# Kernel tuning notes

Measured on AMD Instinct MI355X. Metric: run time of the kernel, lower is better.

The kernel has to match this reference:

```python
import jax, jax.numpy as jnp
import numpy as np

B, L, H, N, CIN, COUT, U = 32, 12, 12, 2048, 2, 1, 64
K3 = 3  # num_matrices = n_supports * max_diffusion_step + 1 = 1*2 + 1


def setup_inputs() -> dict:
    rng = np.random.default_rng(0)
    # random sparse-ish symmetric adjacency -> scaled laplacian support (lambda_max ~= 2)
    A = rng.random((N, N), dtype=np.float32)
    A = np.maximum(A, A.T)
    A = A * (A > 0.995)
    d = A.sum(axis=1)
    dis = 1.0 / np.sqrt(np.maximum(d, 1e-6))
    Lap = np.eye(N, dtype=np.float32) - (dis[:, None] * A) * dis[None, :]
    support = (Lap - np.eye(N, dtype=np.float32)).astype(np.float32)  # 2/lmax*L - I with lmax=2

    key = jax.random.key(0)
    ks = jax.random.split(key, 6)

    def w(k, shape, fan):
        return jax.random.normal(k, shape, jnp.float32) / np.float32(np.sqrt(fan))

    Cg_e = (CIN + U) * K3   # 198
    Cg_d = (COUT + U) * K3  # 195
    return {
        "history_data": jax.random.normal(ks[0], (B, L, N, CIN), jnp.float32),
        "support": jnp.asarray(support),
        "enc_Wg": w(ks[1], (Cg_e, 2 * U), Cg_e),
        "enc_bg": jnp.ones((2 * U,), jnp.float32),  # gate bias starts at 1.0 (original repo)
        "enc_Wc": w(ks[2], (Cg_e, U), Cg_e),
        "enc_bc": jnp.zeros((U,), jnp.float32),
        "dec_Wg": w(ks[3], (Cg_d, 2 * U), Cg_d),
        "dec_bg": jnp.ones((2 * U,), jnp.float32),
        "dec_Wc": w(ks[4], (Cg_d, U), Cg_d),
        "dec_bc": jnp.zeros((U,), jnp.float32),
        "Wp": w(ks[5], (U, COUT), U),
        "bp": jnp.zeros((COUT,), jnp.float32),
    }


def _gconv(support, x, W, b):
    # x: [B, N, C]; Chebyshev diffusion T0=x, T1=Sx, T2=2S(Sx)-x, stacked feature-major
    x1 = jnp.einsum('mn,bnc->bmc', support, x)
    x2 = 2.0 * jnp.einsum('mn,bnc->bmc', support, x1) - x
    xs = jnp.stack([x, x1, x2], axis=-1)  # [B, N, C, 3]
    b_, n_, c_, k_ = xs.shape
    y = xs.reshape(b_ * n_, c_ * k_) @ W + b
    return y.reshape(b_, n_, -1)


def _cell(support, x, h, Wg, bg, Wc, bc):
    # DCGRU cell: x [B,N,in], h [B,N,U]
    cat = jnp.concatenate([x, h], axis=-1)
    ru = jax.nn.sigmoid(_gconv(support, cat, Wg, bg))
    r, u = jnp.split(ru, 2, axis=-1)
    c = jnp.tanh(_gconv(support, jnp.concatenate([x, r * h], axis=-1), Wc, bc))
    return u * h + (1.0 - u) * c


def reference(history_data, support, enc_Wg, enc_bg, enc_Wc, enc_bc,
              dec_Wg, dec_bg, dec_Wc, dec_bc, Wp, bp):
    hist = jnp.transpose(history_data, (1, 0, 2, 3))  # [L, B, N, CIN]
    h0 = jnp.zeros((B, N, U), history_data.dtype)

    def enc_step(h, xt):
        return _cell(support, xt, h, enc_Wg, enc_bg, enc_Wc, enc_bc), None

    h_enc, _ = jax.lax.scan(enc_step, h0, hist)

    go = jnp.zeros((B, N, COUT), history_data.dtype)

    def dec_step(carry, _):
        h, xin = carry
        h = _cell(support, xin, h, dec_Wg, dec_bg, dec_Wc, dec_bc)
        out = (h.reshape(-1, U) @ Wp + bp).reshape(B, N, COUT)
        return (h, out), out

    _, outs = jax.lax.scan(dec_step, (h_enc, go), None, length=H)  # [H, B, N, COUT]
    return jnp.transpose(outs, (1, 0, 2, 3))  # [B, H, N, COUT]
```

## Files before the change

### kernel.cpp

```cpp
#include <hip/hip_runtime.h>
#include <math.h>

#define NN 2048
#define BB 32
#define LL 12
#define HHH 12
#define UU 64
#define STR 68
#define SLAB (BB*STR)
#define SEGS 8
#define SEGW (SLAB/SEGS)
#define MR (NN*BB)
#define CSR_CAP 262144
#define PACK_HALF 28672

typedef short bfrag __attribute__((ext_vector_type(8)));
typedef float ffrag __attribute__((ext_vector_type(4)));

__device__ __forceinline__ float sigm(float x) { return 1.0f / (1.0f + __expf(-x)); }
__device__ __forceinline__ float tanhfast(float x) {
  float e = __expf(2.0f * x);
  return 1.0f - 2.0f / (e + 1.0f);
}

__device__ __forceinline__ void cvt8(const float* a, bfrag* hi, bfrag* lo) {
  bfrag H, L;
  #pragma unroll
  for (int j = 0; j < 8; ++j) {
    unsigned u = __float_as_uint(a[j]);
    unsigned hb = (u + 0x7FFFu + ((u >> 16) & 1u)) >> 16;
    float rem = a[j] - __uint_as_float(hb << 16);
    unsigned u2 = __float_as_uint(rem);
    unsigned lb = (u2 + 0x7FFFu + ((u2 >> 16) & 1u)) >> 16;
    H[j] = (short)hb; L[j] = (short)lb;
  }
  *hi = H; *lo = L;
}

__global__ __launch_bounds__(256) void k_row_count(const float* __restrict__ S, int* __restrict__ cnt) {
  int m = blockIdx.x;
  const float* row = S + (size_t)m * NN;
  int c = 0;
  for (int i = threadIdx.x; i < NN; i += 256) c += (row[i] != 0.0f);
  __shared__ int sm[4];
  for (int off = 32; off; off >>= 1) c += __shfl_down(c, off, 64);
  if ((threadIdx.x & 63) == 0) sm[threadIdx.x >> 6] = c;
  __syncthreads();
  if (threadIdx.x == 0) cnt[m] = sm[0] + sm[1] + sm[2] + sm[3];
}

__global__ __launch_bounds__(256) void k_scan(const int* __restrict__ cnt, int* __restrict__ rp) {
  __shared__ int tot[256];
  int t = threadIdx.x;
  int base = t * 8;
  int v[8]; int s = 0;
  #pragma unroll
  for (int k = 0; k < 8; ++k) { v[k] = cnt[base + k]; s += v[k]; }
  tot[t] = s;
  __syncthreads();
  for (int off = 1; off < 256; off <<= 1) {
    int add = (t >= off) ? tot[t - off] : 0;
    __syncthreads();
    tot[t] += add;
    __syncthreads();
  }
  int run = (t == 0) ? 0 : tot[t - 1];
  #pragma unroll
  for (int k = 0; k < 8; ++k) { rp[base + k] = run; run += v[k]; }
  if (t == 255) rp[NN] = run;
}

__global__ __launch_bounds__(256) void k_fill(const float* __restrict__ S, const int* __restrict__ rp,
                                              int* __restrict__ cols, float* __restrict__ vals) {
  int m = blockIdx.x;
  const float* row = S + (size_t)m * NN;
  __shared__ int wsum[4];
  __shared__ int chunkbase;
  if (threadIdx.x == 0) chunkbase = rp[m];
  __syncthreads();
  int lane = threadIdx.x & 63, w = threadIdx.x >> 6;
  for (int ch = 0; ch < NN / 256; ++ch) {
    int i = ch * 256 + threadIdx.x;
    float val = row[i];
    bool p = (val != 0.0f);
    unsigned long long mask = __ballot(p);
    int rank = __popcll(mask & ((1ull << lane) - 1ull));
    if (lane == 0) wsum[w] = __popcll(mask);
    __syncthreads();
    int off = 0;
    for (int q = 0; q < w; ++q) off += wsum[q];
    if (p) { int k = chunkbase + off + rank; cols[k] = i * SLAB; vals[k] = val; }
    __syncthreads();
    if (threadIdx.x == 0) chunkbase += wsum[0] + wsum[1] + wsum[2] + wsum[3];
    __syncthreads();
  }
}

__global__ __launch_bounds__(256) void k_pack(const float* __restrict__ Wsrc, unsigned short* __restrict__ dst,
                                              int CIN_, int NO) {
  int idx = blockIdx.x * 256 + threadIdx.x;
  int nh_count = NO >> 6;
  int tot = nh_count * 7 * 4 * 64 * 8;
  if (idx >= tot) return;
  int j = idx & 7;
  int r1 = idx >> 3;  int lane = r1 & 63;
  int r2 = r1 >> 6;   int nf = r2 & 3;
  int r3 = r2 >> 2;   int ks = r3 % 7; int nh = r3 / 7;
  int grp = lane >> 4, l15 = lane & 15;
  int col = nh*64 + nf*16 + l15;
  float wv = 0.0f;
  int kb = -1, c = 0;
  if (ks < 6) {
    kb = ks >> 1;
    c = CIN_ + (ks & 1)*32 + grp*8 + j;
  } else {
    int q = grp*8 + j;
    if (q < 3*CIN_) { kb = q / CIN_; c = q % CIN_; }
  }
  if (kb >= 0) {
    float w0 = Wsrc[((size_t)c*3 + 0)*NO + col];
    float w1 = Wsrc[((size_t)c*3 + 1)*NO + col];
    float w2 = Wsrc[((size_t)c*3 + 2)*NO + col];
    wv = (kb == 0) ? (w0 - w2) : ((kb == 1) ? w1 : 2.0f*w2);
  }
  unsigned u = __float_as_uint(wv);
  unsigned hb = (u + 0x7FFFu + ((u >> 16) & 1u)) >> 16;
  float rem = wv - __uint_as_float(hb << 16);
  unsigned u2 = __float_as_uint(rem);
  unsigned lb = (u2 + 0x7FFFu + ((u2 >> 16) & 1u)) >> 16;
  size_t basehi = ((size_t)nh*PACK_HALF) + ((((size_t)ks*4 + nf)*2 + 0)*64 + lane)*8 + j;
  size_t baselo = ((size_t)nh*PACK_HALF) + ((((size_t)ks*4 + nf)*2 + 1)*64 + lane)*8 + j;
  dst[basehi] = (unsigned short)hb;
  dst[baselo] = (unsigned short)lb;
}

__global__ __launch_bounds__(256) void k_setx(const float* __restrict__ hist, float* __restrict__ cat, int t) {
  int idx = blockIdx.x * 256 + threadIdx.x;
  if (idx >= MR * 2) return;
  int c = idx & 1, row = idx >> 1;
  int n = row >> 5, b = row & 31;
  cat[(size_t)row * STR + 64 + c] = hist[(((size_t)(b * LL + t)) * NN + n) * 2 + c];
}

__global__ __launch_bounds__(320) void k_hop(
    const int* __restrict__ rp, const int* __restrict__ colsS, const float* __restrict__ vals,
    const float* __restrict__ src, float* __restrict__ Y) {
  int orig = blockIdx.x;
  int swz = (orig & 7) * 2048 + (orig >> 3);
  int seg = swz >> 11;
  int node = swz & 2047;
  int tid = threadIdx.x;
  if (tid >= SEGW) return;
  int w0 = seg * SEGW + tid;
  int j0 = rp[node], j1 = rp[node + 1];
  float acc0 = 0.f, acc1 = 0.f;
  int j = j0;
  for (; j + 4 <= j1; j += 4) {
    int   o0 = colsS[j],   o1 = colsS[j+1], o2 = colsS[j+2], o3 = colsS[j+3];
    float s0 = vals[j],    s1 = vals[j+1],  s2 = vals[j+2],  s3 = vals[j+3];
    float v0 = src[o0 + w0];
    float v1 = src[o1 + w0];
    float v2 = src[o2 + w0];
    float v3 = src[o3 + w0];
    acc0 = fmaf(s0, v0, acc0);
    acc1 = fmaf(s1, v1, acc1);
    acc0 = fmaf(s2, v2, acc0);
    acc1 = fmaf(s3, v3, acc1);
  }
  for (; j < j1; ++j) acc0 = fmaf(vals[j], src[colsS[j] + w0], acc0);
  Y[(size_t)node * SLAB + w0] = acc0 + acc1;
}

template<int CATM>
__global__ __launch_bounds__(256, 4) void k_gate(
    const float* __restrict__ catP, const float* __restrict__ T1P, const float* __restrict__ T2P,
    const unsigned short* __restrict__ Bpack, const float* __restrict__ bg,
    float* __restrict__ zP, float* __restrict__ Ug) {
  int tid = threadIdx.x;
  int r0 = blockIdx.x * 64;
  int w = tid >> 6, lane = tid & 63, grp = lane >> 4, l15 = lane & 15;
  int row0 = r0 + w*16 + l15;
  ffrag acc[8];
  #pragma unroll
  for (int nf = 0; nf < 8; ++nf) acc[nf] = (ffrag){0.f, 0.f, 0.f, 0.f};

  #pragma unroll
  for (int ks = 0; ks < 7; ++ks) {
    int ko = (ks & 1)*32 + grp*8;
    float av[8] = {0,0,0,0,0,0,0,0};
    if (ks < 6) {
      const float* p0 = (ks < 2) ? catP : ((ks < 4) ? T1P : T2P);
      const float* a0 = p0 + (size_t)row0*STR + ko;
      *(float4*)(av)     = *(const float4*)a0;
      *(float4*)(av + 4) = *(const float4*)(a0 + 4);
    } else if (grp == 0) {
      size_t rb = (size_t)row0*STR + 64;
      if (CATM == 1) {
        av[0] = catP[rb];  av[1] = catP[rb + 1];
        av[2] = T1P[rb];   av[3] = T1P[rb + 1];
        av[4] = T2P[rb];   av[5] = T2P[rb + 1];
      } else {
        av[0] = catP[rb];
        av[1] = T1P[rb];
        av[2] = T2P[rb];
      }
    }
    bfrag ah0, al0;
    cvt8(av, &ah0, &al0);
    #pragma unroll
    for (int nf = 0; nf < 8; ++nf) {
      const unsigned short* bb = Bpack + (size_t)(nf >> 2)*PACK_HALF
                               + (((size_t)(ks*4 + (nf & 3))*2)*64 + lane)*8;
      bfrag bh = *(const bfrag*)bb;
      bfrag bl = *(const bfrag*)(bb + 512);
      acc[nf] = __builtin_amdgcn_mfma_f32_16x16x32_bf16(ah0, bh, acc[nf], 0, 0, 0);
      acc[nf] = __builtin_amdgcn_mfma_f32_16x16x32_bf16(ah0, bl, acc[nf], 0, 0, 0);
      acc[nf] = __builtin_amdgcn_mfma_f32_16x16x32_bf16(al0, bh, acc[nf], 0, 0, 0);
    }
  }
  float bgv[8];
  #pragma unroll
  for (int nf = 0; nf < 8; ++nf) bgv[nf] = bg[nf*16 + l15];
  #pragma unroll
  for (int reg = 0; reg < 4; ++reg) {
    int row = r0 + w*16 + grp*4 + reg;
    #pragma unroll
    for (int nf = 0; nf < 8; ++nf) {
      int col = nf*16 + l15;
      float v = sigm(acc[nf][reg] + bgv[nf]);
      if (col < 64) {
        float ho = catP[(size_t)row*STR + col];
        zP[(size_t)row*STR + col] = v * ho;
      } else {
        Ug[(size_t)row*UU + (col - 64)] = v;
      }
    }
  }
  if (l15 == 0) {
    #pragma unroll
    for (int reg = 0; reg < 4; ++reg) {
      int row = r0 + w*16 + grp*4 + reg;
      size_t zb = (size_t)row*STR;
      zP[zb + 64] = catP[zb + 64];
      zP[zb + 65] = (CATM == 1) ? catP[zb + 65] : 0.f;
      zP[zb + 66] = 0.f; zP[zb + 67] = 0.f;
    }
  }
}

template<bool DEC>
__global__ __launch_bounds__(256, 4) void k_cand(
    const float* __restrict__ zP, const float* __restrict__ T1P, const float* __restrict__ T2P,
    const unsigned short* __restrict__ Bpack, const float* __restrict__ bc,
    const float* __restrict__ Ug, const float* __restrict__ catCur,
    float* __restrict__ catNext,
    const float* __restrict__ Wp, const float* __restrict__ bp,
    float* __restrict__ out, int t) {
  int tid = threadIdx.x;
  int r0 = blockIdx.x * 64;
  int w = tid >> 6, lane = tid & 63, grp = lane >> 4, l15 = lane & 15;
  int row0 = r0 + w*16 + l15;
  ffrag acc[4];
  #pragma unroll
  for (int nf = 0; nf < 4; ++nf) acc[nf] = (ffrag){0.f, 0.f, 0.f, 0.f};

  #pragma unroll
  for (int ks = 0; ks < 7; ++ks) {
    int ko = (ks & 1)*32 + grp*8;
    float av[8] = {0,0,0,0,0,0,0,0};
    if (ks < 6) {
      const float* p0 = (ks < 2) ? zP : ((ks < 4) ? T1P : T2P);
      const float* a0 = p0 + (size_t)row0*STR + ko;
      *(float4*)(av)     = *(const float4*)a0;
      *(float4*)(av + 4) = *(const float4*)(a0 + 4);
    } else if (grp == 0) {
      size_t rb = (size_t)row0*STR + 64;
      if (!DEC) {
        av[0] = zP[rb];  av[1] = zP[rb + 1];
        av[2] = T1P[rb]; av[3] = T1P[rb + 1];
        av[4] = T2P[rb]; av[5] = T2P[rb + 1];
      } else {
        av[0] = zP[rb];
        av[1] = T1P[rb];
        av[2] = T2P[rb];
      }
    }
    bfrag ah0, al0;
    cvt8(av, &ah0, &al0);
    #pragma unroll
    for (int nf = 0; nf < 4; ++nf) {
      const unsigned short* bb = Bpack + (((size_t)(ks*4 + nf)*2)*64 + lane)*8;
      bfrag bh = *(const bfrag*)bb;
      bfrag bl = *(const bfrag*)(bb + 512);
      acc[nf] = __builtin_amdgcn_mfma_f32_16x16x32_bf16(ah0, bh, acc[nf], 0, 0, 0);
      acc[nf] = __builtin_amdgcn_mfma_f32_16x16x32_bf16(ah0, bl, acc[nf], 0, 0, 0);
      acc[nf] = __builtin_amdgcn_mfma_f32_16x16x32_bf16(al0, bh, acc[nf], 0, 0, 0);
    }
  }
  float bcv[4], wpv[4];
  #pragma unroll
  for (int nf = 0; nf < 4; ++nf) {
    bcv[nf] = bc[nf*16 + l15];
    wpv[nf] = DEC ? Wp[nf*16 + l15] : 0.f;
  }
  float bp0 = DEC ? bp[0] : 0.f;
  #pragma unroll
  for (int reg = 0; reg < 4; ++reg) {
    int row = r0 + w*16 + grp*4 + reg;
    float p = 0.f;
    #pragma unroll
    for (int nf = 0; nf < 4; ++nf) {
      int col = nf*16 + l15;
      float cf = tanhfast(acc[nf][reg] + bcv[nf]);
      float u  = Ug[(size_t)row*UU + col];
      float ho = catCur[(size_t)row*STR + col];
      float hv = u * ho + (1.0f - u) * cf;
      catNext[(size_t)row*STR + col] = hv;
      if (DEC) p = fmaf(hv, wpv[nf], p);
    }
    if (DEC) {
      p += __shfl_xor(p, 1, 64);
      p += __shfl_xor(p, 2, 64);
      p += __shfl_xor(p, 4, 64);
      p += __shfl_xor(p, 8, 64);
      if (l15 == 0) {
        float val = p + bp0;
        int n = row >> 5, b = row & 31;
        out[((size_t)b*HHH + t)*NN + n] = val;
        catNext[(size_t)row*STR + 64] = val;
        catNext[(size_t)row*STR + 65] = 0.f;
      }
    } else {
      if (l15 == 0) {
        catNext[(size_t)row*STR + 64] = 0.f;
        catNext[(size_t)row*STR + 65] = 0.f;
      }
    }
  }
}

extern "C" void kernel_launch(void* const* d_in, const int* in_sizes, int n_in,
                              void* d_out, int out_size, void* d_ws, size_t ws_size,
                              hipStream_t stream) {
  (void)in_sizes; (void)n_in; (void)out_size; (void)ws_size;
  const float* hist = (const float*)d_in[0];
  const float* support = (const float*)d_in[1];
  const float* eWg = (const float*)d_in[2];
  const float* ebg = (const float*)d_in[3];
  const float* eWc = (const float*)d_in[4];
  const float* ebc = (const float*)d_in[5];
  const float* dWg = (const float*)d_in[6];
  const float* dbg = (const float*)d_in[7];
  const float* dWc = (const float*)d_in[8];
  const float* dbc = (const float*)d_in[9];
  const float* Wp  = (const float*)d_in[10];
  const float* bp  = (const float*)d_in[11];
  float* out = (float*)d_out;

  char* base = (char*)d_ws;
  size_t off = 0;
  auto carve = [&](size_t bytes) -> void* {
    void* p = base + off;
    off += (bytes + 255) & ~(size_t)255;
    return p;
  };
  int*   cnt   = (int*)carve(NN * 4);
  int*   rpB   = (int*)carve((NN + 1) * 4);
  int*   colsB = (int*)carve(CSR_CAP * 4);
  float* valsB = (float*)carve(CSR_CAP * 4);
  unsigned short* Pge = (unsigned short*)carve(2 * PACK_HALF * 2);
  unsigned short* Pgd = (unsigned short*)carve(2 * PACK_HALF * 2);
  unsigned short* Pce = (unsigned short*)carve((size_t)PACK_HALF * 2);
  unsigned short* Pcd = (unsigned short*)carve((size_t)PACK_HALF * 2);
  float* T1P  = (float*)carve((size_t)NN * SLAB * 4);
  float* T2P  = (float*)carve((size_t)NN * SLAB * 4);
  float* zP   = (float*)carve((size_t)NN * SLAB * 4);
  float* UgF  = (float*)carve((size_t)MR * UU * 4);
  float* catA = (float*)carve((size_t)NN * SLAB * 4);
  float* catB = (float*)carve((size_t)NN * SLAB * 4);

  hipMemsetAsync(catA, 0, (size_t)NN * SLAB * 4, stream);
  hipMemsetAsync(catB, 0, (size_t)NN * SLAB * 4, stream);

  k_row_count<<<NN, 256, 0, stream>>>(support, cnt);
  k_scan<<<1, 256, 0, stream>>>(cnt, rpB);
  k_fill<<<NN, 256, 0, stream>>>(support, rpB, colsB, valsB);
  k_pack<<<112, 256, 0, stream>>>(eWg, Pge, 2, 128);
  k_pack<<<56, 256, 0, stream>>>(eWc, Pce, 2, 64);
  k_pack<<<112, 256, 0, stream>>>(dWg, Pgd, 1, 128);
  k_pack<<<56, 256, 0, stream>>>(dWc, Pcd, 1, 64);

  float* hc = catA; float* hn = catB;
  for (int t = 0; t < LL; ++t) {
    k_setx<<<(MR*2 + 255)/256, 256, 0, stream>>>(hist, hc, t);
    k_hop<<<NN*SEGS, 320, 0, stream>>>(rpB, colsB, valsB, hc, T1P);
    k_hop<<<NN*SEGS, 320, 0, stream>>>(rpB, colsB, valsB, T1P, T2P);
    k_gate<1><<<MR/64, 256, 0, stream>>>(hc, T1P, T2P, Pge, ebg, zP, UgF);
    k_hop<<<NN*SEGS, 320, 0, stream>>>(rpB, colsB, valsB, zP, T1P);
    k_hop<<<NN*SEGS, 320, 0, stream>>>(rpB, colsB, valsB, T1P, T2P);
    k_cand<false><<<MR/64, 256, 0, stream>>>(zP, T1P, T2P, Pce, ebc, UgF, hc, hn,
                                             Wp, bp, out, t);
    float* tmp = hc; hc = hn; hn = tmp;
  }
  for (int t = 0; t < HHH; ++t) {
    k_hop<<<NN*SEGS, 320, 0, stream>>>(rpB, colsB, valsB, hc, T1P);
    k_hop<<<NN*SEGS, 320, 0, stream>>>(rpB, colsB, valsB, T1P, T2P);
    k_gate<2><<<MR/64, 256, 0, stream>>>(hc, T1P, T2P, Pgd, dbg, zP, UgF);
    k_hop<<<NN*SEGS, 320, 0, stream>>>(rpB, colsB, valsB, zP, T1P);
    k_hop<<<NN*SEGS, 320, 0, stream>>>(rpB, colsB, valsB, T1P, T2P);
    k_cand<true><<<MR/64, 256, 0, stream>>>(zP, T1P, T2P, Pcd, dbc, UgF, hc, hn,
                                            Wp, bp, out, t);
    float* tmp = hc; hc = hn; hn = tmp;
  }
}
```

Before: 4.489 ms.

## Stage weights in LDS, split gate columns, pair nodes in hop, fuse setx

The gate and candidate GEMM kernels now copy the packed bf16 weight halves into shared memory once per 512-thread block, and the gate kernel splits its 128 output columns across two blocks. Each hop block now processes two nodes, with their gather loops interleaved. The per-step input-copy kernel is removed: the encoder candidate kernel writes the next step's history features directly. Together these aim to cut global weight re-reads, launch count and per-block overhead, at the cost of a 56KB LDS footprint that limits occupancy and more imbalanced hop work.

```diff
diff --git a/kernel.cpp b/kernel.cpp
--- a/kernel.cpp
+++ b/kernel.cpp
@@ -146,43 +146,72 @@
     const int* __restrict__ rp, const int* __restrict__ colsS, const float* __restrict__ vals,
     const float* __restrict__ src, float* __restrict__ Y) {
   int orig = blockIdx.x;
-  int swz = (orig & 7) * 2048 + (orig >> 3);
-  int seg = swz >> 11;
-  int node = swz & 2047;
+  int seg = orig & 7;
+  int pair = orig >> 3;
+  int nodeA = pair * 2, nodeB = nodeA + 1;
   int tid = threadIdx.x;
   if (tid >= SEGW) return;
   int w0 = seg * SEGW + tid;
-  int j0 = rp[node], j1 = rp[node + 1];
-  float acc0 = 0.f, acc1 = 0.f;
-  int j = j0;
-  for (; j + 4 <= j1; j += 4) {
-    int   o0 = colsS[j],   o1 = colsS[j+1], o2 = colsS[j+2], o3 = colsS[j+3];
-    float s0 = vals[j],    s1 = vals[j+1],  s2 = vals[j+2],  s3 = vals[j+3];
-    float v0 = src[o0 + w0];
-    float v1 = src[o1 + w0];
-    float v2 = src[o2 + w0];
-    float v3 = src[o3 + w0];
-    acc0 = fmaf(s0, v0, acc0);
-    acc1 = fmaf(s1, v1, acc1);
-    acc0 = fmaf(s2, v2, acc0);
-    acc1 = fmaf(s3, v3, acc1);
-  }
-  for (; j < j1; ++j) acc0 = fmaf(vals[j], src[colsS[j] + w0], acc0);
-  Y[(size_t)node * SLAB + w0] = acc0 + acc1;
+  int ja = rp[nodeA], ja1 = rp[nodeA + 1];
+  int jb = rp[nodeB], jb1 = rp[nodeB + 1];
+  float accA0 = 0.f, accA1 = 0.f, accB0 = 0.f, accB1 = 0.f;
+
+  while (ja + 4 <= ja1 && jb + 4 <= jb1) {
+    int   oa0 = colsS[ja],   oa1 = colsS[ja+1], oa2 = colsS[ja+2], oa3 = colsS[ja+3];
+    int   ob0 = colsS[jb],   ob1 = colsS[jb+1], ob2 = colsS[jb+2], ob3 = colsS[jb+3];
+    float sa0 = vals[ja],    sa1 = vals[ja+1],  sa2 = vals[ja+2],  sa3 = vals[ja+3];
+    float sb0 = vals[jb],    sb1 = vals[jb+1],  sb2 = vals[jb+2],  sb3 = vals[jb+3];
+    float va0 = src[oa0 + w0], va1 = src[oa1 + w0], va2 = src[oa2 + w0], va3 = src[oa3 + w0];
+    float vb0 = src[ob0 + w0], vb1 = src[ob1 + w0], vb2 = src[ob2 + w0], vb3 = src[ob3 + w0];
+    accA0 = fmaf(sa0, va0, accA0); accA1 = fmaf(sa1, va1, accA1);
+    accA0 = fmaf(sa2, va2, accA0); accA1 = fmaf(sa3, va3, accA1);
+    accB0 = fmaf(sb0, vb0, accB0); accB1 = fmaf(sb1, vb1, accB1);
+    accB0 = fmaf(sb2, vb2, accB0); accB1 = fmaf(sb3, vb3, accB1);
+    ja += 4; jb += 4;
+  }
+  for (; ja + 4 <= ja1; ja += 4) {
+    int   o0 = colsS[ja],  o1 = colsS[ja+1], o2 = colsS[ja+2], o3 = colsS[ja+3];
+    float s0 = vals[ja],   s1 = vals[ja+1],  s2 = vals[ja+2],  s3 = vals[ja+3];
+    float v0 = src[o0 + w0], v1 = src[o1 + w0], v2 = src[o2 + w0], v3 = src[o3 + w0];
+    accA0 = fmaf(s0, v0, accA0); accA1 = fmaf(s1, v1, accA1);
+    accA0 = fmaf(s2, v2, accA0); accA1 = fmaf(s3, v3, accA1);
+  }
+  for (; ja < ja1; ++ja) accA0 = fmaf(vals[ja], src[colsS[ja] + w0], accA0);
+  for (; jb + 4 <= jb1; jb += 4) {
+    int   o0 = colsS[jb],  o1 = colsS[jb+1], o2 = colsS[jb+2], o3 = colsS[jb+3];
+    float s0 = vals[jb],   s1 = vals[jb+1],  s2 = vals[jb+2],  s3 = vals[jb+3];
+    float v0 = src[o0 + w0], v1 = src[o1 + w0], v2 = src[o2 + w0], v3 = src[o3 + w0];
+    accB0 = fmaf(s0, v0, accB0); accB1 = fmaf(s1, v1, accB1);
+    accB0 = fmaf(s2, v2, accB0); accB1 = fmaf(s3, v3, accB1);
+  }
+  for (; jb < jb1; ++jb) accB0 = fmaf(vals[jb], src[colsS[jb] + w0], accB0);
+
+  Y[(size_t)nodeA * SLAB + w0] = accA0 + accA1;
+  Y[(size_t)nodeB * SLAB + w0] = accB0 + accB1;
 }
 
 template<int CATM>
-__global__ __launch_bounds__(256, 4) void k_gate(
+__global__ __launch_bounds__(512, 4) void k_gate(
     const float* __restrict__ catP, const float* __restrict__ T1P, const float* __restrict__ T2P,
     const unsigned short* __restrict__ Bpack, const float* __restrict__ bg,
     float* __restrict__ zP, float* __restrict__ Ug) {
+  __shared__ __align__(16) unsigned short Bl[PACK_HALF];
   int tid = threadIdx.x;
-  int r0 = blockIdx.x * 64;
+  int bid = blockIdx.x;
+  int nfh = bid & 1;
+  int r0 = (bid >> 1) * 128;
+  {
+    const float4* srcv = (const float4*)(Bpack + (size_t)nfh * PACK_HALF);
+    float4* dstv = (float4*)Bl;
+    #pragma unroll
+    for (int i = 0; i < PACK_HALF/8/512; ++i) dstv[tid + 512*i] = srcv[tid + 512*i];
+  }
+  __syncthreads();
   int w = tid >> 6, lane = tid & 63, grp = lane >> 4, l15 = lane & 15;
   int row0 = r0 + w*16 + l15;
-  ffrag acc[8];
-  #pragma unroll
-  for (int nf = 0; nf < 8; ++nf) acc[nf] = (ffrag){0.f, 0.f, 0.f, 0.f};
+  ffrag acc[4];
+  #pragma unroll
+  for (int nf = 0; nf < 4; ++nf) acc[nf] = (ffrag){0.f, 0.f, 0.f, 0.f};
 
   #pragma unroll
   for (int ks = 0; ks < 7; ++ks) {
@@ -208,9 +237,8 @@
     bfrag ah0, al0;
     cvt8(av, &ah0, &al0);
     #pragma unroll
-    for (int nf = 0; nf < 8; ++nf) {
-      const unsigned short* bb = Bpack + (size_t)(nf >> 2)*PACK_HALF
-                               + (((size_t)(ks*4 + (nf & 3))*2)*64 + lane)*8;
+    for (int nf = 0; nf < 4; ++nf) {
+      const unsigned short* bb = Bl + (((size_t)(ks*4 + nf)*2)*64 + lane)*8;
       bfrag bh = *(const bfrag*)bb;
       bfrag bl = *(const bfrag*)(bb + 512);
       acc[nf] = __builtin_amdgcn_mfma_f32_16x16x32_bf16(ah0, bh, acc[nf], 0, 0, 0);
@@ -218,25 +246,25 @@
       acc[nf] = __builtin_amdgcn_mfma_f32_16x16x32_bf16(al0, bh, acc[nf], 0, 0, 0);
     }
   }
-  float bgv[8];
-  #pragma unroll
-  for (int nf = 0; nf < 8; ++nf) bgv[nf] = bg[nf*16 + l15];
+  float bgv[4];
+  #pragma unroll
+  for (int nf = 0; nf < 4; ++nf) bgv[nf] = bg[nfh*64 + nf*16 + l15];
   #pragma unroll
   for (int reg = 0; reg < 4; ++reg) {
     int row = r0 + w*16 + grp*4 + reg;
     #pragma unroll
-    for (int nf = 0; nf < 8; ++nf) {
+    for (int nf = 0; nf < 4; ++nf) {
       int col = nf*16 + l15;
       float v = sigm(acc[nf][reg] + bgv[nf]);
-      if (col < 64) {
+      if (nfh == 0) {
         float ho = catP[(size_t)row*STR + col];
         zP[(size_t)row*STR + col] = v * ho;
       } else {
-        Ug[(size_t)row*UU + (col - 64)] = v;
+        Ug[(size_t)row*UU + col] = v;
       }
     }
   }
-  if (l15 == 0) {
+  if (nfh == 0 && l15 == 0) {
     #pragma unroll
     for (int reg = 0; reg < 4; ++reg) {
       int row = r0 + w*16 + grp*4 + reg;
@@ -249,15 +277,23 @@
 }
 
 template<bool DEC>
-__global__ __launch_bounds__(256, 4) void k_cand(
+__global__ __launch_bounds__(512, 4) void k_cand(
     const float* __restrict__ zP, const float* __restrict__ T1P, const float* __restrict__ T2P,
     const unsigned short* __restrict__ Bpack, const float* __restrict__ bc,
     const float* __restrict__ Ug, const float* __restrict__ catCur,
     float* __restrict__ catNext,
     const float* __restrict__ Wp, const float* __restrict__ bp,
-    float* __restrict__ out, int t) {
+    float* __restrict__ out, const float* __restrict__ hist, int tpar) {
+  __shared__ __align__(16) unsigned short Bl[PACK_HALF];
   int tid = threadIdx.x;
-  int r0 = blockIdx.x * 64;
+  int r0 = blockIdx.x * 128;
+  {
+    const float4* srcv = (const float4*)Bpack;
+    float4* dstv = (float4*)Bl;
+    #pragma unroll
+    for (int i = 0; i < PACK_HALF/8/512; ++i) dstv[tid + 512*i] = srcv[tid + 512*i];
+  }
+  __syncthreads();
   int w = tid >> 6, lane = tid & 63, grp = lane >> 4, l15 = lane & 15;
   int row0 = r0 + w*16 + l15;
   ffrag acc[4];
@@ -289,7 +325,7 @@
     cvt8(av, &ah0, &al0);
     #pragma unroll
     for (int nf = 0; nf < 4; ++nf) {
-      const unsigned short* bb = Bpack + (((size_t)(ks*4 + nf)*2)*64 + lane)*8;
+      const unsigned short* bb = Bl + (((size_t)(ks*4 + nf)*2)*64 + lane)*8;
       bfrag bh = *(const bfrag*)bb;
       bfrag bl = *(const bfrag*)(bb + 512);
       acc[nf] = __builtin_amdgcn_mfma_f32_16x16x32_bf16(ah0, bh, acc[nf], 0, 0, 0);
@@ -326,14 +362,17 @@
       if (l15 == 0) {
         float val = p + bp0;
         int n = row >> 5, b = row & 31;
-        out[((size_t)b*HHH + t)*NN + n] = val;
+        out[((size_t)b*HHH + tpar)*NN + n] = val;
         catNext[(size_t)row*STR + 64] = val;
         catNext[(size_t)row*STR + 65] = 0.f;
       }
     } else {
       if (l15 == 0) {
-        catNext[(size_t)row*STR + 64] = 0.f;
-        catNext[(size_t)row*STR + 65] = 0.f;
+        int n = row >> 5, b = row & 31;
+        bool hv2 = tpar < LL;
+        const float* hx = hist + (((size_t)(b*LL + tpar)) * NN + n) * 2;
+        catNext[(size_t)row*STR + 64] = hv2 ? hx[0] : 0.f;
+        catNext[(size_t)row*STR + 65] = hv2 ? hx[1] : 0.f;
       }
     }
   }
@@ -389,27 +428,27 @@
   k_pack<<<56, 256, 0, stream>>>(eWc, Pce, 2, 64);
   k_pack<<<112, 256, 0, stream>>>(dWg, Pgd, 1, 128);
   k_pack<<<56, 256, 0, stream>>>(dWc, Pcd, 1, 64);
+  k_setx<<<(MR*2 + 255)/256, 256, 0, stream>>>(hist, catA, 0);
 
   float* hc = catA; float* hn = catB;
   for (int t = 0; t < LL; ++t) {
-    k_setx<<<(MR*2 + 255)/256, 256, 0, stream>>>(hist, hc, t);
-    k_hop<<<NN*SEGS, 320, 0, stream>>>(rpB, colsB, valsB, hc, T1P);
-    k_hop<<<NN*SEGS, 320, 0, stream>>>(rpB, colsB, valsB, T1P, T2P);
-    k_gate<1><<<MR/64, 256, 0, stream>>>(hc, T1P, T2P, Pge, ebg, zP, UgF);
-    k_hop<<<NN*SEGS, 320, 0, stream>>>(rpB, colsB, valsB, zP, T1P);
-    k_hop<<<NN*SEGS, 320, 0, stream>>>(rpB, colsB, valsB, T1P, T2P);
-    k_cand<false><<<MR/64, 256, 0, stream>>>(zP, T1P, T2P, Pce, ebc, UgF, hc, hn,
-                                             Wp, bp, out, t);
+    k_hop<<<NN*SEGS/2, 320, 0, stream>>>(rpB, colsB, valsB, hc, T1P);
+    k_hop<<<NN*SEGS/2, 320, 0, stream>>>(rpB, colsB, valsB, T1P, T2P);
+    k_gate<1><<<MR/128*2, 512, 0, stream>>>(hc, T1P, T2P, Pge, ebg, zP, UgF);
+    k_hop<<<NN*SEGS/2, 320, 0, stream>>>(rpB, colsB, valsB, zP, T1P);
+    k_hop<<<NN*SEGS/2, 320, 0, stream>>>(rpB, colsB, valsB, T1P, T2P);
+    k_cand<false><<<MR/128, 512, 0, stream>>>(zP, T1P, T2P, Pce, ebc, UgF, hc, hn,
+                                              Wp, bp, out, hist, t + 1);
     float* tmp = hc; hc = hn; hn = tmp;
   }
   for (int t = 0; t < HHH; ++t) {
-    k_hop<<<NN*SEGS, 320, 0, stream>>>(rpB, colsB, valsB, hc, T1P);
-    k_hop<<<NN*SEGS, 320, 0, stream>>>(rpB, colsB, valsB, T1P, T2P);
-    k_gate<2><<<MR/64, 256, 0, stream>>>(hc, T1P, T2P, Pgd, dbg, zP, UgF);
-    k_hop<<<NN*SEGS, 320, 0, stream>>>(rpB, colsB, valsB, zP, T1P);
-    k_hop<<<NN*SEGS, 320, 0, stream>>>(rpB, colsB, valsB, T1P, T2P);
-    k_cand<true><<<MR/64, 256, 0, stream>>>(zP, T1P, T2P, Pcd, dbc, UgF, hc, hn,
-                                            Wp, bp, out, t);
+    k_hop<<<NN*SEGS/2, 320, 0, stream>>>(rpB, colsB, valsB, hc, T1P);
+    k_hop<<<NN*SEGS/2, 320, 0, stream>>>(rpB, colsB, valsB, T1P, T2P);
+    k_gate<2><<<MR/128*2, 512, 0, stream>>>(hc, T1P, T2P, Pgd, dbg, zP, UgF);
+    k_hop<<<NN*SEGS/2, 320, 0, stream>>>(rpB, colsB, valsB, zP, T1P);
+    k_hop<<<NN*SEGS/2, 320, 0, stream>>>(rpB, colsB, valsB, T1P, T2P);
+    k_cand<true><<<MR/128, 512, 0, stream>>>(zP, T1P, T2P, Pcd, dbc, UgF, hc, hn,
+                                             Wp, bp, out, hist, t);
     float* tmp = hc; hc = hn; hn = tmp;
   }
 }
```

After: 4.028 ms. 1.11x faster.
